# Optimization experiments

Hardware: AMD Instinct MI355X
Metric: run time of the kernel (lower is better)

Reference implementation:

```python
import jax, jax.numpy as jnp
import numpy as np

N_NODES = 100000
N_EDGES = 3200000
IN_DIM = 128
HIDDEN = 128
NUM_GRAPHS = 512


def setup_inputs() -> dict:
    key = jax.random.key(0)
    ks = jax.random.split(key, 12)
    x = jax.random.normal(ks[0], (N_NODES, IN_DIM), dtype=jnp.float32)
    edge_index = jax.random.randint(ks[1], (2, N_EDGES), 0, N_NODES, dtype=jnp.int64)
    edge_attr = jax.random.normal(ks[2], (N_EDGES, 4), dtype=jnp.float32)
    batch = jnp.sort(jax.random.randint(ks[3], (N_NODES,), 0, NUM_GRAPHS, dtype=jnp.int64))

    def glorot(k, fin, fout):
        s = np.float32(np.sqrt(2.0 / (fin + fout)))
        return jax.random.normal(k, (fin, fout), dtype=jnp.float32) * s

    W0 = glorot(ks[4], IN_DIM, HIDDEN); b0 = jnp.zeros((HIDDEN,), jnp.float32)
    W1 = glorot(ks[5], HIDDEN, HIDDEN); b1 = jnp.zeros((HIDDEN,), jnp.float32)
    W2 = glorot(ks[6], HIDDEN, HIDDEN); b2 = jnp.zeros((HIDDEN,), jnp.float32)
    Wm0 = glorot(ks[7], HIDDEN, HIDDEN); bm0 = jnp.zeros((HIDDEN,), jnp.float32)
    Wm1 = glorot(ks[8], HIDDEN, 1); bm1 = jnp.zeros((1,), jnp.float32)
    return {"x": x, "edge_index": edge_index, "edge_attr": edge_attr, "batch": batch,
            "W0": W0, "b0": b0, "W1": W1, "b1": b1, "W2": W2, "b2": b2,
            "Wm0": Wm0, "bm0": bm0, "Wm1": Wm1, "bm1": bm1}


def reference(x, edge_index, edge_attr, batch, W0, b0, W1, b1, W2, b2, Wm0, bm0, Wm1, bm1):
    # edge_attr is accepted but unused, matching the original GCNConv call.
    N = x.shape[0]
    row = edge_index[0]
    col = edge_index[1]
    # PyG gcn_norm: add self-loops, deg from target index (col), symmetric norm.
    loop = jnp.arange(N, dtype=row.dtype)
    row = jnp.concatenate([row, loop])
    col = jnp.concatenate([col, loop])
    deg = jax.ops.segment_sum(jnp.ones(row.shape, jnp.float32), col, num_segments=N)
    dis = jnp.where(deg > 0, jax.lax.rsqrt(jnp.maximum(deg, 1.0)), 0.0)
    norm = dis[row] * dis[col]  # [E+N]

    def gcn_conv(h, W, b):
        h = h @ W                                  # [N, H] transform first (PyG order)
        msg = h[row] * norm[:, None]               # gather + scale, [E+N, H]
        agg = jax.ops.segment_sum(msg, col, num_segments=N)  # scatter-add
        return agg + b

    h = jax.nn.relu(gcn_conv(x, W0, b0))  # dropout inactive in eval mode
    h = jax.nn.relu(gcn_conv(h, W1, b1))
    h = jax.nn.relu(gcn_conv(h, W2, b2))

    # global_mean_pool: segment mean over graph ids
    sums = jax.ops.segment_sum(h, batch, num_segments=NUM_GRAPHS)
    cnt = jax.ops.segment_sum(jnp.ones((N,), jnp.float32), batch, num_segments=NUM_GRAPHS)
    g = sums / jnp.maximum(cnt, 1.0)[:, None]      # [G, H]

    g = jax.nn.relu(g @ Wm0 + bm0)
    return g @ Wm1 + bm1                           # [G, 1]
```

## Files before the change

kernel.cpp:

```cpp
#include <hip/hip_runtime.h>
#include <hip/hip_fp16.h>


#define HID 128
#define NGR 512
#define NB_SHIFT 9
#define NB_W 512
#define EPB 4096

typedef __attribute__((ext_vector_type(8))) _Float16 half8;
typedef __attribute__((ext_vector_type(4))) float floatx4;


__global__ __launch_bounds__(256) void k_hist(const int* __restrict__ col,
                                              int* __restrict__ ghist, int E, int nb) {
    __shared__ int h[256];
    h[threadIdx.x] = 0;
    __syncthreads();
    for (int e = blockIdx.x * 256 + threadIdx.x; e < E; e += gridDim.x * 256)
        atomicAdd(&h[col[e] >> NB_SHIFT], 1);
    __syncthreads();
    int t = threadIdx.x;
    if (t < nb && h[t]) atomicAdd(&ghist[t], h[t]);
}

__global__ __launch_bounds__(256) void k_bscan(const int* __restrict__ ghist,
                                               int* __restrict__ bbase,
                                               int* __restrict__ rowptr,
                                               int N, int E, int nb) {
    __shared__ int wsum[4];
    int t = threadIdx.x, lane = t & 63, wid = t >> 6;
    int v = (t < nb) ? ghist[t] : 0;
    int sc = v;
    #pragma unroll
    for (int off = 1; off < 64; off <<= 1) {
        int u = __shfl_up(sc, off);
        if (lane >= off) sc += u;
    }
    if (lane == 63) wsum[wid] = sc;
    __syncthreads();
    int offs = 0;
    for (int w = 0; w < wid; w++) offs += wsum[w];
    int excl = offs + sc - v;
    if (t <= nb) bbase[t] = excl;
    if (t == 0) rowptr[N] = E;
}

__global__ __launch_bounds__(512) void k_scatter(const int* __restrict__ row,
                                                 const int* __restrict__ col,
                                                 const int* __restrict__ bbase,
                                                 int* __restrict__ bcur,
                                                 unsigned* __restrict__ sorted, int E) {
    __shared__ int hist[256];
    __shared__ int cur[256];
    int t = threadIdx.x;
    if (t < 256) hist[t] = 0;
    __syncthreads();
    int base = blockIdx.x * EPB;
    #pragma unroll
    for (int i = 0; i < EPB / 512; i++) {
        int e = base + i * 512 + t;
        if (e < E) atomicAdd(&hist[col[e] >> NB_SHIFT], 1);
    }
    __syncthreads();
    if (t < 256 && hist[t] > 0) cur[t] = atomicAdd(&bcur[t], hist[t]);
    __syncthreads();
    #pragma unroll
    for (int i = 0; i < EPB / 512; i++) {
        int e = base + i * 512 + t;
        if (e < E) {
            int d = col[e], b = d >> NB_SHIFT;
            int p = atomicAdd(&cur[b], 1);
            sorted[bbase[b] + p] = ((unsigned)row[e] << NB_SHIFT) | (unsigned)(d & (NB_W - 1));
        }
    }
}

__global__ __launch_bounds__(512) void k_build(const unsigned* __restrict__ sorted,
                                               const int* __restrict__ bbase,
                                               int* __restrict__ csr_src,
                                               int* __restrict__ rowptr,
                                               float* __restrict__ dis, int N) {
    __shared__ int cnt[NB_W];
    __shared__ int excl[NB_W];
    __shared__ int wsum[8];
    int b = blockIdx.x, t = threadIdx.x;
    cnt[t] = 0;
    __syncthreads();
    int s0 = bbase[b], s1 = bbase[b + 1];
    for (int p = s0 + t; p < s1; p += 512)
        atomicAdd(&cnt[sorted[p] & (NB_W - 1)], 1);
    __syncthreads();
    int v = cnt[t];
    int lane = t & 63, wid = t >> 6;
    int sc = v;
    #pragma unroll
    for (int off = 1; off < 64; off <<= 1) {
        int u = __shfl_up(sc, off);
        if (lane >= off) sc += u;
    }
    if (lane == 63) wsum[wid] = sc;
    __syncthreads();
    int offs = 0;
    for (int w = 0; w < wid; w++) offs += wsum[w];
    int e0 = offs + sc - v;
    excl[t] = e0;
    int d = (b << NB_SHIFT) + t;
    if (d < N) { rowptr[d] = s0 + e0; dis[d] = rsqrtf((float)(v + 1)); }
    __syncthreads();
    for (int p = s0 + t; p < s1; p += 512) {
        unsigned sd = sorted[p];
        int q = atomicAdd(&excl[sd & (NB_W - 1)], 1);
        csr_src[s0 + q] = (int)(sd >> NB_SHIFT);
    }
}


__global__ __launch_bounds__(256) void k_wprep(const float* __restrict__ W0,
                                               const float* __restrict__ W1,
                                               const float* __restrict__ W2,
                                               _Float16* __restrict__ Wt) {
    int l = blockIdx.x >> 4;
    int chunk = blockIdx.x & 15;
    const float* W = (l == 0) ? W0 : (l == 1) ? W1 : W2;
    _Float16* D = Wt + (size_t)l * HID * HID;
    int t = threadIdx.x;
    int k  = chunk * 8 + (t >> 5);
    int n0 = (t & 31) * 4;
    float4 v = *(const float4*)(W + (size_t)k * HID + n0);
    D[(size_t)(n0 + 0) * HID + k] = (_Float16)v.x;
    D[(size_t)(n0 + 1) * HID + k] = (_Float16)v.y;
    D[(size_t)(n0 + 2) * HID + k] = (_Float16)v.z;
    D[(size_t)(n0 + 3) * HID + k] = (_Float16)v.w;
}


__device__ __forceinline__ half8 load_afrag(const float* A, int arow, int k0, int N) {
    const float* p = A + (size_t)arow * HID + k0;
    float4 v0 = *(const float4*)p;
    float4 v1 = *(const float4*)(p + 4);
    half8 h;
    h[0] = (_Float16)v0.x; h[1] = (_Float16)v0.y;
    h[2] = (_Float16)v0.z; h[3] = (_Float16)v0.w;
    h[4] = (_Float16)v1.x; h[5] = (_Float16)v1.y;
    h[6] = (_Float16)v1.z; h[7] = (_Float16)v1.w;
    return h;
}
__device__ __forceinline__ half8 load_afrag(const _Float16* A, int arow, int k0, int N) {
    return *(const half8*)(A + ((size_t)(k0 >> 6) * N + arow) * 64 + (k0 & 63));
}

template <typename AT>
__global__ __launch_bounds__(256, 2) void k_gemm(const AT* __restrict__ A,
                                                 const _Float16* __restrict__ Wt,
                                                 const float* __restrict__ dis,
                                                 __half* __restrict__ C, int N) {
    const int lane = threadIdx.x & 63;
    const int quad = lane >> 4;
    const int mc   = lane & 15;
    const int gw   = (blockIdx.x * 256 + threadIdx.x) >> 6;
    const int nw   = (gridDim.x * 256) >> 6;
    const int nstrips = (N + 15) >> 4;

    half8 b[8][4];
    #pragma unroll
    for (int j = 0; j < 8; j++)
        #pragma unroll
        for (int s = 0; s < 4; s++)
            b[j][s] = *(const half8*)(Wt + (size_t)(j * 16 + mc) * HID + s * 32 + quad * 8);

    int strip = gw;
    if (strip >= nstrips) return;

    half8 a[4];
    {
        int arow = strip * 16 + mc; if (arow >= N) arow = N - 1;
        #pragma unroll
        for (int s = 0; s < 4; s++) a[s] = load_afrag(A, arow, s * 32 + quad * 8, N);
    }

    for (; strip < nstrips; strip += nw) {
        const int row0 = strip * 16;
        const int next = strip + nw;
        half8 an[4];
        if (next < nstrips) {
            int arow = next * 16 + mc; if (arow >= N) arow = N - 1;
            #pragma unroll
            for (int s = 0; s < 4; s++) an[s] = load_afrag(A, arow, s * 32 + quad * 8, N);
        }
        floatx4 acc[8];
        #pragma unroll
        for (int j = 0; j < 8; j++) acc[j] = (floatx4){0.f, 0.f, 0.f, 0.f};
        #pragma unroll
        for (int s = 0; s < 4; s++)
            #pragma unroll
            for (int j = 0; j < 8; j++)
                acc[j] = __builtin_amdgcn_mfma_f32_16x16x32_f16(a[s], b[j][s], acc[j], 0, 0, 0);
        #pragma unroll
        for (int r = 0; r < 4; r++) {
            int gr = row0 + quad * 4 + r;
            if (gr < N) {
                float ds = dis[gr];
                #pragma unroll
                for (int j = 0; j < 8; j++)
                    C[((size_t)(j >> 2) * N + gr) * 64 + (j & 3) * 16 + mc] =
                        __float2half(ds * acc[j][r]);
            }
        }
        #pragma unroll
        for (int s = 0; s < 4; s++) a[s] = an[s];
    }
}


__device__ __forceinline__ void add8(float* acc, float4 r) {
    __half2* h = (__half2*)&r;
    #pragma unroll
    for (int k = 0; k < 4; k++) {
        float2 v = __half22float2(h[k]);
        acc[2 * k]     += v.x;
        acc[2 * k + 1] += v.y;
    }
}

__global__ __launch_bounds__(256) void k_agg(const __half* __restrict__ T,
                                             const float* __restrict__ dis,
                                             const int* __restrict__ rowptr,
                                             const int* __restrict__ csr_src,
                                             const float* __restrict__ bias,
                                             __half* __restrict__ out, int N) {
    const int b    = blockIdx.x;
    const int pass = (b >> 2) & 1;
    const int nbi  = ((b >> 3) << 2) | (b & 3);
    const int g    = threadIdx.x >> 5;
    const int l    = threadIdx.x & 31;
    const int p    = l >> 3;
    const int h    = l & 7;
    const int n = nbi * 8 + g;
    if (n >= N) return;

    const float4* T4 = (const float4*)(T + (size_t)pass * N * 64);

    float acc[8] = {};

    int e  = rowptr[n];
    int e1 = rowptr[n + 1];
    for (; e + 16 <= e1; e += 16) {
        int s0 = csr_src[e + p];
        int s1 = csr_src[e + 4 + p];
        int s2 = csr_src[e + 8 + p];
        int s3 = csr_src[e + 12 + p];
        float4 r0 = T4[(size_t)s0 * 8 + h];
        float4 r1 = T4[(size_t)s1 * 8 + h];
        float4 r2 = T4[(size_t)s2 * 8 + h];
        float4 r3 = T4[(size_t)s3 * 8 + h];
        add8(acc, r0); add8(acc, r1); add8(acc, r2); add8(acc, r3);
    }
    for (; e + 4 <= e1; e += 4) {
        int s = csr_src[e + p];
        add8(acc, T4[(size_t)s * 8 + h]);
    }
    if (e + p < e1) {
        int s = csr_src[e + p];
        add8(acc, T4[(size_t)s * 8 + h]);
    }
    if (p == 0) add8(acc, T4[(size_t)n * 8 + h]);

    #pragma unroll
    for (int k = 0; k < 8; k++) {
        acc[k] += __shfl_xor(acc[k], 8, 64);
        acc[k] += __shfl_xor(acc[k], 16, 64);
    }

    if (p == 0) {
        float dn = dis[n];
        half8 o;
        #pragma unroll
        for (int k = 0; k < 8; k++) {
            float v = fmaf(dn, acc[k], bias[pass * 64 + h * 8 + k]);
            o[k] = (_Float16)fmaxf(v, 0.f);
        }
        *(half8*)((_Float16*)out + ((size_t)pass * N + n) * 64 + h * 8) = o;
    }
}


__device__ __forceinline__ int lbound(const int* __restrict__ batch, int N, int g) {
    int lo = 0, hi = N;
    while (lo < hi) {
        int mid = (lo + hi) >> 1;
        if (batch[mid] < g) lo = mid + 1; else hi = mid;
    }
    return lo;
}

__global__ __launch_bounds__(256) void k_poolmlp(const __half* __restrict__ hbuf,
                                                 const int* __restrict__ batch,
                                                 const float* __restrict__ Wm0,
                                                 const float* __restrict__ bm0,
                                                 const float* __restrict__ Wm1,
                                                 const float* __restrict__ bm1,
                                                 float* __restrict__ out, int N) {
    __shared__ float red[2048];
    __shared__ float g[HID];
    const int gr = blockIdx.x, t = threadIdx.x;
    const int s = lbound(batch, N, gr), e = lbound(batch, N, gr + 1);

    const int rg = t >> 4, cl = t & 15;
    const _Float16* base = (const _Float16*)hbuf
        + (size_t)(cl >> 3) * N * 64 + (size_t)(cl & 7) * 8;
    float acc[8] = {};
    for (int r = s + rg; r < e; r += 16) {
        half8 v = *(const half8*)(base + (size_t)r * 64);
        #pragma unroll
        for (int k = 0; k < 8; k++) acc[k] += (float)v[k];
    }
    #pragma unroll
    for (int k = 0; k < 8; k++) red[t * 8 + k] = acc[k];
    __syncthreads();
    if (t < 128) {
        int cl2 = t >> 3, k = t & 7;
        float sm = 0.f;
        #pragma unroll
        for (int rg2 = 0; rg2 < 16; rg2++) sm += red[(rg2 * 16 + cl2) * 8 + k];
        int feat = (cl2 & 7) * 8 + k + ((cl2 >> 3) ? 64 : 0);
        g[feat] = sm / fmaxf((float)(e - s), 1.f);
    }
    __syncthreads();

    const int j = t & 127, hh = t >> 7;
    float a = 0.f;
    for (int k = hh * 64; k < hh * 64 + 64; k++)
        a = fmaf(g[k], Wm0[(size_t)k * HID + j], a);
    red[hh * 128 + j] = a;
    __syncthreads();

    if (t < 128) {
        float h1 = fmaxf(bm0[j] + red[j] + red[128 + j], 0.f);
        float z = h1 * Wm1[j];
        #pragma unroll
        for (int off = 32; off > 0; off >>= 1) z += __shfl_xor(z, off, 64);
        if ((t & 63) == 0) red[1024 + (t >> 6)] = z;
    }
    __syncthreads();
    if (t == 0) out[gr] = red[1024] + red[1025] + bm1[0];
}


extern "C" void kernel_launch(void* const* d_in, const int* in_sizes, int n_in,
                              void* d_out, int out_size, void* d_ws, size_t ws_size,
                              hipStream_t stream) {
    const float* x     = (const float*)d_in[0];
    const int*   ei    = (const int*)d_in[1];
    const int*   batch = (const int*)d_in[3];
    const float* W0 = (const float*)d_in[4],  *b0 = (const float*)d_in[5];
    const float* W1 = (const float*)d_in[6],  *b1 = (const float*)d_in[7];
    const float* W2 = (const float*)d_in[8],  *b2 = (const float*)d_in[9];
    const float* Wm0 = (const float*)d_in[10], *bm0 = (const float*)d_in[11];
    const float* Wm1 = (const float*)d_in[12], *bm1 = (const float*)d_in[13];

    const int N = in_sizes[0] / HID;
    const int E = in_sizes[1] / 2;
    const int nb = (N + NB_W - 1) >> NB_SHIFT;
    const int* row  = ei;
    const int* colI = ei + E;

    char* w = (char*)d_ws;
    auto carve = [&](size_t bytes) {
        void* p = (void*)w;
        w += (bytes + 255) & ~(size_t)255;
        return p;
    };
    int*      ibuf    = (int*)     carve(512 * 4);
    int*      bbase   = (int*)     carve(257 * 4);
    float*    dis     = (float*)   carve((size_t)N * 4);
    int*      rowptr  = (int*)     carve((size_t)(N + 1) * 4);
    unsigned* sorted  = (unsigned*)carve((size_t)E * 4);
    int*      csr_src = (int*)     carve((size_t)E * 4);
    _Float16* wth     = (_Float16*)carve((size_t)3 * HID * HID * 2);
    __half*   bufT    = (__half*)  carve((size_t)N * HID * 2);
    __half*   bufA    = (__half*)  carve((size_t)N * HID * 2);
    __half*   bufB    = (__half*)  carve((size_t)N * HID * 2);

    int* ghist = ibuf;
    int* bcur  = ibuf + 256;

    hipMemsetAsync(ibuf, 0, 512 * 4, stream);
    k_wprep  <<<48, 256, 0, stream>>>(W0, W1, W2, wth);
    k_hist   <<<512, 256, 0, stream>>>(colI, ghist, E, nb);
    k_bscan  <<<1, 256, 0, stream>>>(ghist, bbase, rowptr, N, E, nb);
    k_scatter<<<(E + EPB - 1) / EPB, 512, 0, stream>>>(row, colI, bbase, bcur, sorted, E);
    k_build  <<<nb, 512, 0, stream>>>(sorted, bbase, csr_src, rowptr, dis, N);

    dim3 gg(512);
    const int nblk4 = (((N + 7) / 8) + 3) & ~3;
    dim3 ga(2 * nblk4);

    k_gemm<float>    <<<gg, 256, 0, stream>>>(x, wth, dis, bufT, N);
    k_agg            <<<ga, 256, 0, stream>>>(bufT, dis, rowptr, csr_src, b0, bufA, N);
    k_gemm<_Float16> <<<gg, 256, 0, stream>>>((const _Float16*)bufA, wth + HID * HID, dis, bufT, N);
    k_agg            <<<ga, 256, 0, stream>>>(bufT, dis, rowptr, csr_src, b1, bufB, N);
    k_gemm<_Float16> <<<gg, 256, 0, stream>>>((const _Float16*)bufB, wth + 2 * HID * HID, dis, bufT, N);
    k_agg            <<<ga, 256, 0, stream>>>(bufT, dis, rowptr, csr_src, b2, bufA, N);

    k_poolmlp<<<NGR, 256, 0, stream>>>(bufA, batch, Wm0, bm0, Wm1, bm1, (float*)d_out, N);
}
```

Baseline: 629.7 us.

## Split feature buffers into eight 16-wide slabs for aggregation locality

Changes the intermediate activation layout from two 64-feature slabs to eight 16-feature slabs (32 bytes per node per slab). The GEMM store, GEMM A-fragment load, aggregation and pooling indexing are all updated to match. Aggregation now runs 8 passes, each with 32 nodes per block and 8 lanes per node, so the gathered working set per pass is much smaller and fits in cache better. It also switches the csr index loads and output stores to nontemporal hints. The cost is that the edge index list is re-read eight times instead of twice, and each gathered row segment is only 32 bytes.

Result: slower. 1.005 ms (+59.7%).

```diff
diff --git a/kernel.cpp b/kernel.cpp
--- a/kernel.cpp
+++ b/kernel.cpp
@@ -147,7 +147,7 @@
     return h;
 }
 __device__ __forceinline__ half8 load_afrag(const _Float16* A, int arow, int k0, int N) {
-    return *(const half8*)(A + ((size_t)(k0 >> 6) * N + arow) * 64 + (k0 & 63));
+    return *(const half8*)(A + ((size_t)(k0 >> 4) * N + arow) * 16 + (k0 & 15));
 }
 
 template <typename AT>
@@ -203,8 +203,7 @@
                 float ds = dis[gr];
                 #pragma unroll
                 for (int j = 0; j < 8; j++)
-                    C[((size_t)(j >> 2) * N + gr) * 64 + (j & 3) * 16 + mc] =
-                        __float2half(ds * acc[j][r]);
+                    C[((size_t)j * N + gr) * 16 + mc] = __float2half(ds * acc[j][r]);
             }
         }
         #pragma unroll
@@ -230,46 +229,46 @@
                                              const float* __restrict__ bias,
                                              __half* __restrict__ out, int N) {
     const int b    = blockIdx.x;
-    const int pass = (b >> 2) & 1;
-    const int nbi  = ((b >> 3) << 2) | (b & 3);
-    const int g    = threadIdx.x >> 5;
-    const int l    = threadIdx.x & 31;
-    const int p    = l >> 3;
-    const int h    = l & 7;
-    const int n = nbi * 8 + g;
+    const int pass = b & 7;
+    const int nbi  = b >> 3;
+    const int t    = threadIdx.x;
+    const int l    = t & 7;
+    const int p    = l >> 1;
+    const int h    = l & 1;
+    const int n = nbi * 32 + (t >> 3);
     if (n >= N) return;
 
-    const float4* T4 = (const float4*)(T + (size_t)pass * N * 64);
+    const float4* T4 = (const float4*)(T + (size_t)pass * N * 16);
 
     float acc[8] = {};
 
     int e  = rowptr[n];
     int e1 = rowptr[n + 1];
     for (; e + 16 <= e1; e += 16) {
-        int s0 = csr_src[e + p];
-        int s1 = csr_src[e + 4 + p];
-        int s2 = csr_src[e + 8 + p];
-        int s3 = csr_src[e + 12 + p];
-        float4 r0 = T4[(size_t)s0 * 8 + h];
-        float4 r1 = T4[(size_t)s1 * 8 + h];
-        float4 r2 = T4[(size_t)s2 * 8 + h];
-        float4 r3 = T4[(size_t)s3 * 8 + h];
+        int s0 = __builtin_nontemporal_load(csr_src + e + p);
+        int s1 = __builtin_nontemporal_load(csr_src + e + 4 + p);
+        int s2 = __builtin_nontemporal_load(csr_src + e + 8 + p);
+        int s3 = __builtin_nontemporal_load(csr_src + e + 12 + p);
+        float4 r0 = T4[(size_t)s0 * 2 + h];
+        float4 r1 = T4[(size_t)s1 * 2 + h];
+        float4 r2 = T4[(size_t)s2 * 2 + h];
+        float4 r3 = T4[(size_t)s3 * 2 + h];
         add8(acc, r0); add8(acc, r1); add8(acc, r2); add8(acc, r3);
     }
     for (; e + 4 <= e1; e += 4) {
-        int s = csr_src[e + p];
-        add8(acc, T4[(size_t)s * 8 + h]);
+        int s = __builtin_nontemporal_load(csr_src + e + p);
+        add8(acc, T4[(size_t)s * 2 + h]);
     }
     if (e + p < e1) {
-        int s = csr_src[e + p];
-        add8(acc, T4[(size_t)s * 8 + h]);
-    }
-    if (p == 0) add8(acc, T4[(size_t)n * 8 + h]);
+        int s = __builtin_nontemporal_load(csr_src + e + p);
+        add8(acc, T4[(size_t)s * 2 + h]);
+    }
+    if (p == 0) add8(acc, T4[(size_t)n * 2 + h]);
 
     #pragma unroll
     for (int k = 0; k < 8; k++) {
-        acc[k] += __shfl_xor(acc[k], 8, 64);
-        acc[k] += __shfl_xor(acc[k], 16, 64);
+        acc[k] += __shfl_xor(acc[k], 2, 64);
+        acc[k] += __shfl_xor(acc[k], 4, 64);
     }
 
     if (p == 0) {
@@ -277,10 +276,11 @@
         half8 o;
         #pragma unroll
         for (int k = 0; k < 8; k++) {
-            float v = fmaf(dn, acc[k], bias[pass * 64 + h * 8 + k]);
+            float v = fmaf(dn, acc[k], bias[pass * 16 + h * 8 + k]);
             o[k] = (_Float16)fmaxf(v, 0.f);
         }
-        *(half8*)((_Float16*)out + ((size_t)pass * N + n) * 64 + h * 8) = o;
+        __builtin_nontemporal_store(
+            o, (half8*)((_Float16*)out + ((size_t)pass * N + n) * 16 + h * 8));
     }
 }
 
@@ -308,10 +308,10 @@
 
     const int rg = t >> 4, cl = t & 15;
     const _Float16* base = (const _Float16*)hbuf
-        + (size_t)(cl >> 3) * N * 64 + (size_t)(cl & 7) * 8;
+        + (size_t)(cl >> 1) * N * 16 + (size_t)(cl & 1) * 8;
     float acc[8] = {};
     for (int r = s + rg; r < e; r += 16) {
-        half8 v = *(const half8*)(base + (size_t)r * 64);
+        half8 v = *(const half8*)(base + (size_t)r * 16);
         #pragma unroll
         for (int k = 0; k < 8; k++) acc[k] += (float)v[k];
     }
@@ -323,7 +323,7 @@
         float sm = 0.f;
         #pragma unroll
         for (int rg2 = 0; rg2 < 16; rg2++) sm += red[(rg2 * 16 + cl2) * 8 + k];
-        int feat = (cl2 & 7) * 8 + k + ((cl2 >> 3) ? 64 : 0);
+        int feat = (cl2 >> 1) * 16 + (cl2 & 1) * 8 + k;
         g[feat] = sm / fmaxf((float)(e - s), 1.f);
     }
     __syncthreads();
@@ -393,8 +393,8 @@
     k_build  <<<nb, 512, 0, stream>>>(sorted, bbase, csr_src, rowptr, dis, N);
 
     dim3 gg(512);
-    const int nblk4 = (((N + 7) / 8) + 3) & ~3;
-    dim3 ga(2 * nblk4);
+    const int npb = (N + 31) / 32;
+    dim3 ga(8 * npb);
 
     k_gemm<float>    <<<gg, 256, 0, stream>>>(x, wth, dis, bufT, N);
     k_agg            <<<ga, 256, 0, stream>>>(bufT, dis, rowptr, csr_src, b0, bufA, N);
```

## Stage scatter output in LDS for coalesced bucket writes; fuse weight prep with histogram

Applied to the files above, without the earlier changes.

The edge-bucketing scatter kernel now does a block-local counting sort into shared memory, then writes each bucket's run contiguously to global memory instead of issuing random per-edge stores. Column indices are cached in registers so they are read once, and EPB doubles to 8192 so each bucket run is longer. The weight transpose kernel is merged into the histogram kernel to save a launch. In exchange, the kernel uses about 40KB of LDS plus an extra local scan and a serial bmap fill loop, which can lower occupancy.

After: 599.5 us. 1.05x faster.

```diff
diff --git a/kernel.cpp b/kernel.cpp
--- a/kernel.cpp
+++ b/kernel.cpp
@@ -6,18 +6,38 @@
 #define NGR 512
 #define NB_SHIFT 9
 #define NB_W 512
-#define EPB 4096
+#define EPB 8192
 
 typedef __attribute__((ext_vector_type(8))) _Float16 half8;
 typedef __attribute__((ext_vector_type(4))) float floatx4;
 
 
-__global__ __launch_bounds__(256) void k_hist(const int* __restrict__ col,
+__global__ __launch_bounds__(256) void k_prep(const float* __restrict__ W0,
+                                              const float* __restrict__ W1,
+                                              const float* __restrict__ W2,
+                                              _Float16* __restrict__ Wt,
+                                              const int* __restrict__ col,
                                               int* __restrict__ ghist, int E, int nb) {
+    if (blockIdx.x < 48) {
+        int l = blockIdx.x >> 4;
+        int chunk = blockIdx.x & 15;
+        const float* W = (l == 0) ? W0 : (l == 1) ? W1 : W2;
+        _Float16* D = Wt + (size_t)l * HID * HID;
+        int t = threadIdx.x;
+        int k  = chunk * 8 + (t >> 5);
+        int n0 = (t & 31) * 4;
+        float4 v = *(const float4*)(W + (size_t)k * HID + n0);
+        D[(size_t)(n0 + 0) * HID + k] = (_Float16)v.x;
+        D[(size_t)(n0 + 1) * HID + k] = (_Float16)v.y;
+        D[(size_t)(n0 + 2) * HID + k] = (_Float16)v.z;
+        D[(size_t)(n0 + 3) * HID + k] = (_Float16)v.w;
+        return;
+    }
     __shared__ int h[256];
     h[threadIdx.x] = 0;
     __syncthreads();
-    for (int e = blockIdx.x * 256 + threadIdx.x; e < E; e += gridDim.x * 256)
+    const int nblk = gridDim.x - 48;
+    for (int e = (blockIdx.x - 48) * 256 + threadIdx.x; e < E; e += nblk * 256)
         atomicAdd(&h[col[e] >> NB_SHIFT], 1);
     __syncthreads();
     int t = threadIdx.x;
@@ -46,33 +66,79 @@
     if (t == 0) rowptr[N] = E;
 }
 
+
 __global__ __launch_bounds__(512) void k_scatter(const int* __restrict__ row,
                                                  const int* __restrict__ col,
                                                  const int* __restrict__ bbase,
                                                  int* __restrict__ bcur,
                                                  unsigned* __restrict__ sorted, int E) {
     __shared__ int hist[256];
+    __shared__ int lofs[256];
     __shared__ int cur[256];
-    int t = threadIdx.x;
+    __shared__ int gbase[256];
+    __shared__ int wsum[8];
+    __shared__ unsigned stage[EPB];
+    __shared__ unsigned char bmap[EPB];
+
+    const int t = threadIdx.x;
+    const int base = blockIdx.x * EPB;
     if (t < 256) hist[t] = 0;
     __syncthreads();
-    int base = blockIdx.x * EPB;
-    #pragma unroll
-    for (int i = 0; i < EPB / 512; i++) {
-        int e = base + i * 512 + t;
-        if (e < E) atomicAdd(&hist[col[e] >> NB_SHIFT], 1);
-    }
-    __syncthreads();
-    if (t < 256 && hist[t] > 0) cur[t] = atomicAdd(&bcur[t], hist[t]);
-    __syncthreads();
+
+    int dcache[EPB / 512];
     #pragma unroll
     for (int i = 0; i < EPB / 512; i++) {
         int e = base + i * 512 + t;
         if (e < E) {
-            int d = col[e], b = d >> NB_SHIFT;
+            int d = col[e];
+            dcache[i] = d;
+            atomicAdd(&hist[d >> NB_SHIFT], 1);
+        } else dcache[i] = -1;
+    }
+    __syncthreads();
+
+    int v = (t < 256) ? hist[t] : 0;
+    int lane = t & 63, wid = t >> 6;
+    int sc = v;
+    #pragma unroll
+    for (int off = 1; off < 64; off <<= 1) {
+        int u = __shfl_up(sc, off);
+        if (lane >= off) sc += u;
+    }
+    if (lane == 63) wsum[wid] = sc;
+    __syncthreads();
+    int offs = 0;
+    for (int w = 0; w < wid; w++) offs += wsum[w];
+    int e0 = offs + sc - v;
+    if (t < 256) {
+        lofs[t] = e0;
+        cur[t]  = e0;
+        if (hist[t] > 0) gbase[t] = atomicAdd(&bcur[t], hist[t]);
+    }
+    __syncthreads();
+
+    if (t < 256) {
+        int c = hist[t], b0 = lofs[t];
+        for (int k = 0; k < c; k++) bmap[b0 + k] = (unsigned char)t;
+    }
+    __syncthreads();
+
+    #pragma unroll
+    for (int i = 0; i < EPB / 512; i++) {
+        int e = base + i * 512 + t;
+        if (e < E) {
+            int d = dcache[i];
+            int b = d >> NB_SHIFT;
             int p = atomicAdd(&cur[b], 1);
-            sorted[bbase[b] + p] = ((unsigned)row[e] << NB_SHIFT) | (unsigned)(d & (NB_W - 1));
+            stage[p] = ((unsigned)row[e] << NB_SHIFT) | (unsigned)(d & (NB_W - 1));
         }
+    }
+    __syncthreads();
+
+    int valid = E - base; if (valid > EPB) valid = EPB;
+    for (int j = t; j < valid; j += 512) {
+        int b = bmap[j];
+        sorted[bbase[b] + gbase[b] + (j - lofs[b])] = stage[j];
     }
 }
 
@@ -113,25 +179,6 @@
         int q = atomicAdd(&excl[sd & (NB_W - 1)], 1);
         csr_src[s0 + q] = (int)(sd >> NB_SHIFT);
     }
-}
-
-
-__global__ __launch_bounds__(256) void k_wprep(const float* __restrict__ W0,
-                                               const float* __restrict__ W1,
-                                               const float* __restrict__ W2,
-                                               _Float16* __restrict__ Wt) {
-    int l = blockIdx.x >> 4;
-    int chunk = blockIdx.x & 15;
-    const float* W = (l == 0) ? W0 : (l == 1) ? W1 : W2;
-    _Float16* D = Wt + (size_t)l * HID * HID;
-    int t = threadIdx.x;
-    int k  = chunk * 8 + (t >> 5);
-    int n0 = (t & 31) * 4;
-    float4 v = *(const float4*)(W + (size_t)k * HID + n0);
-    D[(size_t)(n0 + 0) * HID + k] = (_Float16)v.x;
-    D[(size_t)(n0 + 1) * HID + k] = (_Float16)v.y;
-    D[(size_t)(n0 + 2) * HID + k] = (_Float16)v.z;
-    D[(size_t)(n0 + 3) * HID + k] = (_Float16)v.w;
 }
 
 
@@ -386,8 +433,7 @@
     int* bcur  = ibuf + 256;
 
     hipMemsetAsync(ibuf, 0, 512 * 4, stream);
-    k_wprep  <<<48, 256, 0, stream>>>(W0, W1, W2, wth);
-    k_hist   <<<512, 256, 0, stream>>>(colI, ghist, E, nb);
+    k_prep   <<<48 + 512, 256, 0, stream>>>(W0, W1, W2, wth, colI, ghist, E, nb);
     k_bscan  <<<1, 256, 0, stream>>>(ghist, bbase, rowptr, N, E, nb);
     k_scatter<<<(E + EPB - 1) / EPB, 512, 0, stream>>>(row, colI, bbase, bcur, sorted, E);
     k_build  <<<nb, 512, 0, stream>>>(sorted, bbase, csr_src, rowptr, dis, N);
```
